# Performance work log

Hardware: AMD Instinct MI355X
Metric: run time of the kernel (lower is better)

The kernel has to match this reference:

```python
import jax, jax.numpy as jnp
import numpy as np

T, B, V, NG, H, MLP = 1024, 128, 128, 10, 1024, 128
F = V + NG  # feature_size = alphabet one-hot + genre one-hot


def setup_inputs() -> dict:
    key = jax.random.key(0)
    ks = jax.random.split(key, 14)
    s = 0.02
    inp = {
        "x": jax.random.normal(ks[0], (T, B, F), dtype=jnp.float32),
        # LSTMCell 1: input F -> hidden H (PyTorch layout: W_ih [4H, F], W_hh [4H, H])
        "W_ih1": jax.random.normal(ks[1], (4 * H, F), dtype=jnp.float32) * s,
        "b_ih1": jax.random.normal(ks[2], (4 * H,), dtype=jnp.float32) * s,
        "W_hh1": jax.random.normal(ks[3], (4 * H, H), dtype=jnp.float32) * s,
        "b_hh1": jax.random.normal(ks[4], (4 * H,), dtype=jnp.float32) * s,
        # LSTMCell 2: H -> H
        "W_ih2": jax.random.normal(ks[5], (4 * H, H), dtype=jnp.float32) * s,
        "b_ih2": jax.random.normal(ks[6], (4 * H,), dtype=jnp.float32) * s,
        "W_hh2": jax.random.normal(ks[7], (4 * H, H), dtype=jnp.float32) * s,
        "b_hh2": jax.random.normal(ks[8], (4 * H,), dtype=jnp.float32) * s,
        # MLP head: Linear(H,128) -> SELU -> Linear(128, V). Dropout(0.2) is identity in eval.
        "W1": jax.random.normal(ks[9], (MLP, H), dtype=jnp.float32) * s,
        "b1": jax.random.normal(ks[10], (MLP,), dtype=jnp.float32) * s,
        "W2": jax.random.normal(ks[11], (V, MLP), dtype=jnp.float32) * s,
        "b2": jax.random.normal(ks[12], (V,), dtype=jnp.float32) * s,
        "predict": 0,
    }
    return inp


def _lstm_cell(xt, h, c, W_ih, b_ih, W_hh, b_hh):
    # PyTorch LSTMCell gate order: input, forget, cell(g), output
    gates = xt @ W_ih.T + b_ih + h @ W_hh.T + b_hh  # [B, 4H]
    i, f, g, o = jnp.split(gates, 4, axis=-1)
    i, f, o = jax.nn.sigmoid(i), jax.nn.sigmoid(f), jax.nn.sigmoid(o)
    g = jnp.tanh(g)
    c_new = f * c + i * g
    h_new = o * jnp.tanh(c_new)
    return h_new, c_new


def reference(x, W_ih1, b_ih1, W_hh1, b_hh1, W_ih2, b_ih2, W_hh2, b_hh2,
              W1, b1, W2, b2, predict):
    n = x.shape[1]
    h0 = jnp.zeros((n, H), dtype=jnp.float32)
    init = (h0, h0, h0, h0)  # h_t, c_t, h2_t, c2_t

    def step(carry, xt):
        h, c, h2, c2 = carry
        h, c = _lstm_cell(xt, h, c, W_ih1, b_ih1, W_hh1, b_hh1)
        h2, c2 = _lstm_cell(h, h2, c2, W_ih2, b_ih2, W_hh2, b_hh2)
        out = jax.nn.selu(h2 @ W1.T + b1) @ W2.T + b2  # [B, V]
        return (h, c, h2, c2), out

    _, outputs = jax.lax.scan(step, init, x)  # [T, B, V]
    return outputs
```

## Files before the change

### kernel.cpp

```cpp
#include <hip/hip_runtime.h>
#include <cstdint>
#include <cstddef>

#define TT   1024
#define BB   128
#define FEAT 138
#define FPAD 160
#define HH   1024
#define VV   128
#define MM   128
#define K1   1184
#define K1P  1280
#define K2   2048
#define HCH  1024
#define H1N  131072
#define MIDN 16384
#define PKM1 1032
#define PKM2 136
#define OFF_RED 0
#define OFF_WM  32768
#define OFF_H   65792
#define OFF_M   67840
#define LDSZ    68864

typedef __bf16 bf16x8 __attribute__((ext_vector_type(8)));
typedef float  f32x4  __attribute__((ext_vector_type(4)));
typedef unsigned short u16;

__device__ __forceinline__ u16 f2bf(float f) {
  uint32_t u = __float_as_uint(f);
  u += 0x7fffu + ((u >> 16) & 1u);
  return (u16)(u >> 16);
}
__device__ __forceinline__ float sigm(float x) { return 1.0f / (1.0f + __expf(-x)); }
__device__ __forceinline__ float tanh_(float x) {
  float e = __expf(-2.0f * fabsf(x));
  float t = (1.0f - e) / (1.0f + e);
  return x < 0.0f ? -t : t;
}

__device__ __forceinline__ bf16x8 ldcc8(const u16* p) {
  union { unsigned long long q[2]; bf16x8 v; } u;
  const unsigned long long* p64 = (const unsigned long long*)p;
  u.q[0] = __hip_atomic_load(p64,     __ATOMIC_RELAXED, __HIP_MEMORY_SCOPE_AGENT);
  u.q[1] = __hip_atomic_load(p64 + 1, __ATOMIC_RELAXED, __HIP_MEMORY_SCOPE_AGENT);
  return u.v;
}
__device__ __forceinline__ void stcc16(u16* p, uint4 v) {
  unsigned long long* p64 = (unsigned long long*)p;
  unsigned long long lo = ((unsigned long long)v.y << 32) | v.x;
  unsigned long long hi = ((unsigned long long)v.w << 32) | v.z;
  __hip_atomic_store(p64,     lo, __ATOMIC_RELAXED, __HIP_MEMORY_SCOPE_AGENT);
  __hip_atomic_store(p64 + 1, hi, __ATOMIC_RELAXED, __HIP_MEMORY_SCOPE_AGENT);
}

__global__ void conv_w1i(const float* __restrict__ Wih, const float* __restrict__ Whh,
                         const float* __restrict__ bi, const float* __restrict__ bh,
                         u16* __restrict__ dst, float* __restrict__ bsum) {
  int rp = blockIdx.x;
  int hc = rp >> 2, g = rp & 3;
  int sr = g * HH + hc;
  if (threadIdx.x == 0) bsum[rp] = bi[sr] + bh[sr];
  for (int k = threadIdx.x; k < K1P; k += 256) {
    float v = 0.0f;
    if (k < FPAD)    v = (k < FEAT) ? Wih[(size_t)sr * FEAT + k] : 0.0f;
    else if (k < K1) v = Whh[(size_t)sr * HH + (k - FPAD)];
    dst[(size_t)rp * K1P + k] = f2bf(v);
  }
}
__global__ void conv_w2i(const float* __restrict__ Wih, const float* __restrict__ Whh,
                         const float* __restrict__ bi, const float* __restrict__ bh,
                         u16* __restrict__ dst, float* __restrict__ bsum) {
  int rp = blockIdx.x;
  int hc = rp >> 2, g = rp & 3;
  int sr = g * HH + hc;
  if (threadIdx.x == 0) bsum[rp] = bi[sr] + bh[sr];
  for (int k = threadIdx.x; k < K2; k += 256) {
    float v = (k < HH) ? Wih[(size_t)sr * HH + k] : Whh[(size_t)sr * HH + (k - HH)];
    dst[(size_t)rp * K2 + k] = f2bf(v);
  }
}
__global__ void conv_mlpw(const float* __restrict__ W1, const float* __restrict__ W2,
                          u16* __restrict__ A, u16* __restrict__ Bm) {
  int i = blockIdx.x * 256 + threadIdx.x;
  if (i < MM * HH) A[i] = f2bf(W1[i]);
  else {
    int j = i - MM * HH;
    if (j < VV * MM) Bm[j] = f2bf(W2[j]);
  }
}
__global__ void conv_x(const float* __restrict__ x, u16* __restrict__ Xb) {
  int blk = blockIdx.x;
  int t = blk / 20, c = blk % 20;
  int b = threadIdx.x;
  if (b >= BB) return;
  const float* src = x + ((size_t)t * BB + b) * FEAT;
  u16 v[8];
#pragma unroll
  for (int e = 0; e < 8; ++e) {
    int col = c * 8 + e;
    v[e] = (col < FEAT) ? f2bf(src[col]) : (u16)0;
  }
  *(uint4*)(Xb + (((size_t)t * 20 + c) * BB + b) * 8) = *(uint4*)v;
}
__global__ void zero_ws(uint4* __restrict__ p, int n16) {
  int i = blockIdx.x * 256 + threadIdx.x;
  if (i < n16) p[i] = uint4{0, 0, 0, 0};
}


__device__ __forceinline__ void mac_step(const bf16x8& a0, const bf16x8& a1,
                                         const u16* __restrict__ bptr,
                                         f32x4 (&acc)[2][4]) {
  bf16x8 Bf[4];
#pragma unroll
  for (int n = 0; n < 4; ++n) Bf[n] = *(const bf16x8*)(bptr + n * 128);
#pragma unroll
  for (int n = 0; n < 4; ++n) {
    acc[0][n] = __builtin_amdgcn_mfma_f32_16x16x32_bf16(a0, Bf[n], acc[0][n], 0, 0, 0);
    acc[1][n] = __builtin_amdgcn_mfma_f32_16x16x32_bf16(a1, Bf[n], acc[1][n], 0, 0, 0);
  }
}

__device__ __forceinline__ void ld_tile_cc(const u16* bptr, bf16x8 (&B)[4]) {
#pragma unroll
  for (int n = 0; n < 4; ++n) B[n] = ldcc8(bptr + n * 128);
}
__device__ __forceinline__ void mfma_tile(const bf16x8& a0, const bf16x8& a1,
                                          const bf16x8 (&B)[4], f32x4 (&acc)[2][4]) {
#pragma unroll
  for (int n = 0; n < 4; ++n) {
    acc[0][n] = __builtin_amdgcn_mfma_f32_16x16x32_bf16(a0, B[n], acc[0][n], 0, 0, 0);
    acc[1][n] = __builtin_amdgcn_mfma_f32_16x16x32_bf16(a1, B[n], acc[1][n], 0, 0, 0);
  }
}
template<int NT, int OFS, int NA>
__device__ __forceinline__ void mac_ring_cc(const bf16x8 (&A0)[NA], const bf16x8 (&A1)[NA],
                                            const u16* __restrict__ bp,
                                            f32x4 (&acc)[2][4]) {
  constexpr int D = NT < 4 ? NT : 4;
  bf16x8 Bq[D][4];
#pragma unroll
  for (int s = 0; s < D; ++s) ld_tile_cc(bp + (size_t)s * 4096, Bq[s]);
#pragma unroll
  for (int s = 0; s < NT; ++s) {
    mfma_tile(A0[OFS + s], A1[OFS + s], Bq[s % D], acc);
    if (s + D < NT) ld_tile_cc(bp + (size_t)(s + D) * 4096, Bq[s % D]);
  }
}

__device__ __forceinline__ void red_write(float* __restrict__ rg,
                                          const f32x4 (&acc)[2][4], int lane) {
#pragma unroll
  for (int mt = 0; mt < 2; ++mt)
#pragma unroll
    for (int n = 0; n < 4; ++n)
      *(f32x4*)(rg + (mt * 4 + n) * 256 + lane * 4) = acc[mt][n];
}
__device__ __forceinline__ void red_add(const float* __restrict__ rg,
                                        f32x4 (&acc)[2][4], int lane) {
#pragma unroll
  for (int mt = 0; mt < 2; ++mt)
#pragma unroll
    for (int n = 0; n < 4; ++n)
      acc[mt][n] += *(const f32x4*)(rg + (mt * 4 + n) * 256 + lane * 4);
}

__device__ __forceinline__ void lstm_tail(f32x4 (&acc)[2][4], const f32x4& bsv0,
                                          const f32x4& bsv1, float (&cst)[2][4],
                                          char* smem, int bh, int lane, int q, int l16,
                                          u16* __restrict__ houtChunk) {
  u16* st = (u16*)(smem + OFF_H) + bh * 512;
#pragma unroll
  for (int mt = 0; mt < 2; ++mt) {
    const f32x4 bsv = mt ? bsv1 : bsv0;
#pragma unroll
    for (int n = 0; n < 4; ++n) {
      float iv = sigm(acc[mt][n][0] + bsv[0]);
      float fv = sigm(acc[mt][n][1] + bsv[1]);
      float gv = tanh_(acc[mt][n][2] + bsv[2]);
      float ov = sigm(acc[mt][n][3] + bsv[3]);
      float c = fv * cst[mt][n] + iv * gv;
      cst[mt][n] = c;
      st[(n * 16 + l16) * 8 + mt * 4 + q] = f2bf(ov * tanh_(c));
    }
  }
  uint4 hv4 = *(uint4*)((u16*)(smem + OFF_H) + bh * 512 + lane * 8);
  stcc16(houtChunk + ((size_t)bh * 64 + lane) * 8, hv4);
}

__device__ __forceinline__ void gbar(unsigned* __restrict__ bar, unsigned g) {
  asm volatile("s_waitcnt vmcnt(0)" ::: "memory");
  __syncthreads();
  if (threadIdx.x == 0) {
    unsigned v = __hip_atomic_fetch_add(&bar[(blockIdx.x & 7) * 16], 1u,
                                        __ATOMIC_RELAXED, __HIP_MEMORY_SCOPE_AGENT);
    if (v == 32u * g - 1u) {
      unsigned w = __hip_atomic_fetch_add(&bar[128], 1u,
                                          __ATOMIC_RELAXED, __HIP_MEMORY_SCOPE_AGENT);
      if (w == 8u * g - 1u)
        __hip_atomic_store(&bar[144], g, __ATOMIC_RELAXED, __HIP_MEMORY_SCOPE_AGENT);
    }
    while (__hip_atomic_load(&bar[144], __ATOMIC_RELAXED,
                             __HIP_MEMORY_SCOPE_AGENT) < g)
      __builtin_amdgcn_s_sleep(8);
  }
  __syncthreads();
}

__global__ __launch_bounds__(512, 2) void fused_lstm(
    const u16* __restrict__ W1i, const u16* __restrict__ W2i,
    const u16* __restrict__ W1m, const u16* __restrict__ W2m,
    const u16* __restrict__ Xb, u16* __restrict__ h1b, u16* __restrict__ h2b,
    u16* __restrict__ midb,
    const float* __restrict__ bs1, const float* __restrict__ bs2,
    const float* __restrict__ bm1, const float* __restrict__ bm2,
    float* __restrict__ out, unsigned* __restrict__ bar)
{
  extern __shared__ char smem[];
  const int tid = threadIdx.x, bid = blockIdx.x;
  const int w = tid >> 6, lane = tid & 63, q = lane >> 4, l16 = lane & 15;
  const int kw = w & 3, bh = w >> 2;
  const bool isL1 = bid < 128;
  const int j = isL1 ? bid : bid - 128;
  float* red = (float*)(smem + OFF_RED);
  u16* Wm = (u16*)(smem + OFF_WM);

  float cst[2][4] = {{0, 0, 0, 0}, {0, 0, 0, 0}};
  f32x4 bsv0 = {0, 0, 0, 0}, bsv1 = {0, 0, 0, 0};
  if (kw == 0) {
    const float* bs = isL1 ? bs1 : bs2;
    bsv0 = *(const f32x4*)(bs + (j * 8 + q) * 4);
    bsv1 = *(const f32x4*)(bs + (j * 8 + 4 + q) * 4);
  }

  if (isL1) {
    bf16x8 A1[2][10];
#pragma unroll
    for (int mt = 0; mt < 2; ++mt)
#pragma unroll
      for (int s = 0; s < 10; ++s)
        A1[mt][s] = *(const bf16x8*)(W1i + (size_t)(j * 32 + mt * 16 + l16) * K1P +
                                     (size_t)(kw * 10 + s) * 32 + q * 8);
    if (j < 64) {
      int m0 = (j & 7) * 16;
      for (int i = tid; i < 16 * 128; i += 512) {
        int r = i >> 7, c8 = i & 127;
        *(uint4*)(Wm + r * PKM1 + c8 * 8) =
            *(const uint4*)(W1m + ((size_t)(m0 + r)) * HH + c8 * 8);
      }
    } else {
      int v0 = ((j - 64) & 7) * 16;
      for (int i = tid; i < 16 * 16; i += 512) {
        int r = i >> 4, c8 = i & 15;
        *(uint4*)(Wm + r * PKM2 + c8 * 8) =
            *(const uint4*)(W2m + ((size_t)(v0 + r)) * MM + c8 * 8);
      }
    }
    f32x4 bmv = {0, 0, 0, 0};
    if (w == 3) {
      if (j < 64) bmv = *(const f32x4*)(bm1 + (j & 7) * 16 + q * 4);
      else        bmv = *(const f32x4*)(bm2 + ((j - 64) & 7) * 16 + q * 4);
    }
    __syncthreads();

    for (int p = 0; p < TT + 3; ++p) {
      const bool act = p < TT;
      if (act) {
        const u16* h1p = h1b + (size_t)((p - 1) & 1) * H1N;
        f32x4 acc[2][4];
#pragma unroll
        for (int mt = 0; mt < 2; ++mt)
#pragma unroll
          for (int n = 0; n < 4; ++n) acc[mt][n] = (f32x4){0, 0, 0, 0};
        if (kw == 0) {
          const u16* bx = Xb + (size_t)p * 20480 +
                          ((size_t)q * 128 + bh * 64 + l16) * 8;
#pragma unroll
          for (int s = 0; s < 5; ++s)
            mac_step(A1[0][s], A1[1][s], bx + (size_t)s * 4096, acc);
          const u16* bp = h1p + ((size_t)q * 128 + bh * 64 + l16) * 8;
          mac_ring_cc<5, 5, 10>(A1[0], A1[1], bp, acc);
        } else {
          const u16* bp = h1p + ((size_t)((kw * 10 - 5) * 4 + q) * 128 +
                                 bh * 64 + l16) * 8;
          mac_ring_cc<10, 0, 10>(A1[0], A1[1], bp, acc);
        }
        if (kw >= 2) red_write(red + (bh * 2 + kw - 2) * 2048, acc, lane);
        __syncthreads();
        if (kw < 2)  red_add(red + (bh * 2 + kw) * 2048, acc, lane);
        if (kw == 1) red_write(red + (bh * 2 + 1) * 2048, acc, lane);
        __syncthreads();
        if (kw == 0) {
          red_add(red + (bh * 2 + 1) * 2048, acc, lane);
          lstm_tail(acc, bsv0, bsv1, cst, smem, bh, lane, q, l16,
                    h1b + (size_t)(p & 1) * H1N + (size_t)j * HCH);
        }
      }
      if (w == 3) {
        if (j < 64) {
          if (p >= 2 && p <= TT + 1) {
            int jm = j & 7, jb = j >> 3;
            const u16* bsrc = h2b + (size_t)(p & 1) * H1N + q * HCH +
                              (jb * 16 + l16) * 8;
            const u16* am = Wm + l16 * PKM1 + q * 8;
            f32x4 acc = {0, 0, 0, 0};
            bf16x8 Bq[8];
#pragma unroll
            for (int s = 0; s < 8; ++s) Bq[s] = ldcc8(bsrc + (size_t)s * 4096);
#pragma unroll
            for (int s = 0; s < 32; ++s) {
              bf16x8 af = *(const bf16x8*)(am + s * 32);
              acc = __builtin_amdgcn_mfma_f32_16x16x32_bf16(af, Bq[s % 8], acc, 0, 0, 0);
              if (s + 8 < 32) Bq[s % 8] = ldcc8(bsrc + (size_t)(s + 8) * 4096);
            }
            const float SC = 1.0507009873554804934193349852946f;
            const float AL = 1.6732632423543772848170429916717f;
            u16* st16 = (u16*)(smem + OFF_M);
#pragma unroll
            for (int r = 0; r < 4; ++r) {
              float v = acc[r] + bmv[r];
              v = v > 0.0f ? SC * v : SC * AL * (__expf(v) - 1.0f);
              st16[l16 * 16 + q * 4 + r] = f2bf(v);
            }
            if (lane < 16) {
              uint4 v0 = *(uint4*)(st16 + lane * 16);
              uint4 v1 = *(uint4*)(st16 + lane * 16 + 8);
              u16* mc = midb + (size_t)(p & 1) * MIDN;
              stcc16(mc + (size_t)(2 * jm) * HCH + (jb * 16 + lane) * 8, v0);
              stcc16(mc + (size_t)(2 * jm + 1) * HCH + (jb * 16 + lane) * 8, v1);
            }
          }
        } else if (p >= 3) {
          int jj = j - 64, jv = jj & 7, jb = jj >> 3;
          const u16* bsrc = midb + (size_t)((p - 3) & 1) * MIDN + q * HCH +
                            (jb * 16 + l16) * 8;
          const u16* am = Wm + l16 * PKM2 + q * 8;
          f32x4 acc = {0, 0, 0, 0};
          bf16x8 Bq[4];
#pragma unroll
          for (int s = 0; s < 4; ++s) Bq[s] = ldcc8(bsrc + (size_t)s * 4096);
#pragma unroll
          for (int s = 0; s < 4; ++s) {
            bf16x8 af = *(const bf16x8*)(am + s * 32);
            acc = __builtin_amdgcn_mfma_f32_16x16x32_bf16(af, Bq[s], acc, 0, 0, 0);
          }
          float* stf = (float*)(smem + OFF_M);
#pragma unroll
          for (int r = 0; r < 4; ++r) stf[l16 * 16 + q * 4 + r] = acc[r] + bmv[r];
          if (lane < 16) {
            float* orow = out + ((size_t)(p - 3) * BB + jb * 16 + lane) * VV + jv * 16;
            uint4* s4 = (uint4*)(stf + lane * 16);
            *(uint4*)(orow + 0)  = s4[0];
            *(uint4*)(orow + 4)  = s4[1];
            *(uint4*)(orow + 8)  = s4[2];
            *(uint4*)(orow + 12) = s4[3];
          }
        }
      }
      gbar(bar, (unsigned)p + 1u);
    }
  } else {
    bf16x8 A2[2][16];
#pragma unroll
    for (int mt = 0; mt < 2; ++mt)
#pragma unroll
      for (int s = 0; s < 16; ++s)
        A2[mt][s] = *(const bf16x8*)(W2i + (size_t)(j * 32 + mt * 16 + l16) * K2 +
                                     (size_t)(kw * 16 + s) * 32 + q * 8);

    for (int p = 0; p < TT + 3; ++p) {
      const bool act = (p >= 1 && p <= TT);
      if (act) {
        const int t = p - 1;
        const u16* h1c = h1b + (size_t)(t & 1) * H1N;
        const u16* h2p = h2b + (size_t)((t - 1) & 1) * H1N;
        const u16* src = (kw < 2) ? h1c : h2p;
        const u16* bbase = src + ((size_t)((kw & 1) * 64 + q) * 128 +
                                  bh * 64 + l16) * 8;
        f32x4 acc[2][4];
#pragma unroll
        for (int mt = 0; mt < 2; ++mt)
#pragma unroll
          for (int n = 0; n < 4; ++n) acc[mt][n] = (f32x4){0, 0, 0, 0};
        mac_ring_cc<16, 0, 16>(A2[0], A2[1], bbase, acc);

        if (kw >= 2) red_write(red + (bh * 2 + kw - 2) * 2048, acc, lane);
        __syncthreads();
        if (kw < 2)  red_add(red + (bh * 2 + kw) * 2048, acc, lane);
        if (kw == 1) red_write(red + (bh * 2 + 1) * 2048, acc, lane);
        __syncthreads();
        if (kw == 0) {
          red_add(red + (bh * 2 + 1) * 2048, acc, lane);
          lstm_tail(acc, bsv0, bsv1, cst, smem, bh, lane, q, l16,
                    h2b + (size_t)(t & 1) * H1N + (size_t)j * HCH);
        }
      }
      gbar(bar, (unsigned)p + 1u);
    }
  }
}

extern "C" void kernel_launch(void* const* d_in, const int* in_sizes, int n_in,
                              void* d_out, int out_size, void* d_ws, size_t ws_size,
                              hipStream_t stream)
{
  const float* x    = (const float*)d_in[0];
  const float* Wih1 = (const float*)d_in[1];
  const float* bih1 = (const float*)d_in[2];
  const float* Whh1 = (const float*)d_in[3];
  const float* bhh1 = (const float*)d_in[4];
  const float* Wih2 = (const float*)d_in[5];
  const float* bih2 = (const float*)d_in[6];
  const float* Whh2 = (const float*)d_in[7];
  const float* bhh2 = (const float*)d_in[8];
  const float* W1   = (const float*)d_in[9];
  const float* b1   = (const float*)d_in[10];
  const float* W2   = (const float*)d_in[11];
  const float* b2   = (const float*)d_in[12];
  float* out = (float*)d_out;
  (void)in_sizes; (void)n_in; (void)out_size;

  char* ws = (char*)d_ws;
  size_t off = 0;
  auto alloc = [&](size_t n) { char* p = ws + off; off += (n + 255) & ~(size_t)255; return p; };
  u16* W1i   = (u16*)alloc((size_t)4096 * K1P * 2);
  u16* W2i   = (u16*)alloc((size_t)4096 * K2 * 2);
  u16* W1m   = (u16*)alloc((size_t)MM * HH * 2);
  u16* W2m   = (u16*)alloc((size_t)VV * MM * 2);
  u16* Xb    = (u16*)alloc((size_t)TT * 20 * BB * 8 * 2);
  float* bs1 = (float*)alloc(4096 * 4);
  float* bs2 = (float*)alloc(4096 * 4);
  u16* h1b   = (u16*)alloc(2 * (size_t)H1N * 2 + 32768);
  u16* h2b   = (u16*)alloc(2 * (size_t)H1N * 2);
  u16* midb  = (u16*)alloc(2 * (size_t)MIDN * 2);
  unsigned* bar = (unsigned*)alloc(4096);
  if (ws_size < off) return;

  conv_w1i<<<4096, 256, 0, stream>>>(Wih1, Whh1, bih1, bhh1, W1i, bs1);
  conv_w2i<<<4096, 256, 0, stream>>>(Wih2, Whh2, bih2, bhh2, W2i, bs2);
  conv_mlpw<<<576, 256, 0, stream>>>(W1, W2, W1m, W2m);
  conv_x<<<TT * 20, 128, 0, stream>>>(x, Xb);
  {
    int n16 = (int)((2 * (size_t)H1N * 2 + 32768 + 2 * (size_t)H1N * 2 +
                     2 * (size_t)MIDN * 2 + 4096) / 16);
    zero_ws<<<(n16 + 255) / 256, 256, 0, stream>>>((uint4*)h1b, n16);
  }

  (void)hipFuncSetAttribute((const void*)fused_lstm,
                            hipFuncAttributeMaxDynamicSharedMemorySize, LDSZ);
  void* args[] = { (void*)&W1i, (void*)&W2i, (void*)&W1m, (void*)&W2m,
                   (void*)&Xb, (void*)&h1b, (void*)&h2b, (void*)&midb,
                   (void*)&bs1, (void*)&bs2, (void*)&b1, (void*)&b2,
                   (void*)&out, (void*)&bar };
  hipError_t err = hipLaunchCooperativeKernel((const void*)fused_lstm,
                                              dim3(256), dim3(512), args, LDSZ, stream);
  if (err != hipSuccess) {
    fused_lstm<<<dim3(256), dim3(512), LDSZ, stream>>>(W1i, W2i, W1m, W2m, Xb,
                                                       h1b, h2b, midb, bs1, bs2,
                                                       b1, b2, out, bar);
  }
}
```

Before: 16.16 ms.

## Replace grid barrier with per-block flag wait over deep ring buffers

Adds a MODE 4 path that replaces the two-level atomic grid barrier with per-block completion flags. Every block polls all 256 flags before each phase, and an acquire fence is issued only once every 128 phases, staggered per block. Hidden-state and MLP intermediate buffers become 256-deep rings with padded strides. Reads that used to be coherent atomic loads become plain vector loads, relying on fresh ring slots so stale cache lines are not hit. The cost is much more workspace, and correctness now depends on the ring depth and the sparse fences. Layer-1 blocks with kw==3 also skip padded K tiles, and the barrier sleep is shortened.

```diff
diff --git a/kernel.cpp b/kernel.cpp
--- a/kernel.cpp
+++ b/kernel.cpp
@@ -15,6 +15,9 @@
 #define HCH  1024
 #define H1N  131072
 #define MIDN 16384
+#define H1S  135168
+#define MIDS 20480
+#define RING 256
 #define PKM1 1032
 #define PKM2 136
 #define OFF_RED 0
@@ -39,13 +42,6 @@
   return x < 0.0f ? -t : t;
 }
 
-__device__ __forceinline__ bf16x8 ldcc8(const u16* p) {
-  union { unsigned long long q[2]; bf16x8 v; } u;
-  const unsigned long long* p64 = (const unsigned long long*)p;
-  u.q[0] = __hip_atomic_load(p64,     __ATOMIC_RELAXED, __HIP_MEMORY_SCOPE_AGENT);
-  u.q[1] = __hip_atomic_load(p64 + 1, __ATOMIC_RELAXED, __HIP_MEMORY_SCOPE_AGENT);
-  return u.v;
-}
 __device__ __forceinline__ void stcc16(u16* p, uint4 v) {
   unsigned long long* p64 = (unsigned long long*)p;
   unsigned long long lo = ((unsigned long long)v.y << 32) | v.x;
@@ -109,23 +105,6 @@
 }
 
 
-__device__ __forceinline__ void mac_step(const bf16x8& a0, const bf16x8& a1,
-                                         const u16* __restrict__ bptr,
-                                         f32x4 (&acc)[2][4]) {
-  bf16x8 Bf[4];
-#pragma unroll
-  for (int n = 0; n < 4; ++n) Bf[n] = *(const bf16x8*)(bptr + n * 128);
-#pragma unroll
-  for (int n = 0; n < 4; ++n) {
-    acc[0][n] = __builtin_amdgcn_mfma_f32_16x16x32_bf16(a0, Bf[n], acc[0][n], 0, 0, 0);
-    acc[1][n] = __builtin_amdgcn_mfma_f32_16x16x32_bf16(a1, Bf[n], acc[1][n], 0, 0, 0);
-  }
-}
-
-__device__ __forceinline__ void ld_tile_cc(const u16* bptr, bf16x8 (&B)[4]) {
-#pragma unroll
-  for (int n = 0; n < 4; ++n) B[n] = ldcc8(bptr + n * 128);
-}
 __device__ __forceinline__ void mfma_tile(const bf16x8& a0, const bf16x8& a1,
                                           const bf16x8 (&B)[4], f32x4 (&acc)[2][4]) {
 #pragma unroll
@@ -134,18 +113,22 @@
     acc[1][n] = __builtin_amdgcn_mfma_f32_16x16x32_bf16(a1, B[n], acc[1][n], 0, 0, 0);
   }
 }
+__device__ __forceinline__ void ld_tile(const u16* __restrict__ p, bf16x8 (&B)[4]) {
+#pragma unroll
+  for (int n = 0; n < 4; ++n) B[n] = *(const bf16x8*)(p + n * 128);
+}
 template<int NT, int OFS, int NA>
-__device__ __forceinline__ void mac_ring_cc(const bf16x8 (&A0)[NA], const bf16x8 (&A1)[NA],
-                                            const u16* __restrict__ bp,
-                                            f32x4 (&acc)[2][4]) {
+__device__ __forceinline__ void mac_ring(const bf16x8 (&A0)[NA], const bf16x8 (&A1)[NA],
+                                         const u16* __restrict__ bp,
+                                         f32x4 (&acc)[2][4]) {
   constexpr int D = NT < 4 ? NT : 4;
   bf16x8 Bq[D][4];
 #pragma unroll
-  for (int s = 0; s < D; ++s) ld_tile_cc(bp + (size_t)s * 4096, Bq[s]);
+  for (int s = 0; s < D; ++s) ld_tile(bp + (size_t)s * 4096, Bq[s]);
 #pragma unroll
   for (int s = 0; s < NT; ++s) {
     mfma_tile(A0[OFS + s], A1[OFS + s], Bq[s % D], acc);
-    if (s + D < NT) ld_tile_cc(bp + (size_t)(s + D) * 4096, Bq[s % D]);
+    if (s + D < NT) ld_tile(bp + (size_t)(s + D) * 4096, Bq[s % D]);
   }
 }
 
@@ -187,6 +170,30 @@
   }
   uint4 hv4 = *(uint4*)((u16*)(smem + OFF_H) + bh * 512 + lane * 8);
   stcc16(houtChunk + ((size_t)bh * 64 + lane) * 8, hv4);
+}
+
+template<int MODE>
+__device__ __forceinline__ void wait_phase(const int* __restrict__ F, int p, int lane,
+                                           bool dofence) {
+  if (threadIdx.x < 64) {
+    if (dofence)
+      __builtin_amdgcn_fence(__ATOMIC_ACQUIRE, "agent");
+    for (;;) {
+      int a = __hip_atomic_load(F + lane,       __ATOMIC_RELAXED, __HIP_MEMORY_SCOPE_AGENT);
+      int b = __hip_atomic_load(F + 64 + lane,  __ATOMIC_RELAXED, __HIP_MEMORY_SCOPE_AGENT);
+      int c = __hip_atomic_load(F + 128 + lane, __ATOMIC_RELAXED, __HIP_MEMORY_SCOPE_AGENT);
+      int d = __hip_atomic_load(F + 192 + lane, __ATOMIC_RELAXED, __HIP_MEMORY_SCOPE_AGENT);
+      if (__all(a >= p && b >= p && c >= p && d >= p)) break;
+      __builtin_amdgcn_s_sleep(1);
+    }
+  }
+  __syncthreads();
+}
+__device__ __forceinline__ void done_phase(int* __restrict__ slot, int p) {
+  asm volatile("s_waitcnt vmcnt(0)" ::: "memory");
+  __syncthreads();
+  if (threadIdx.x == 0)
+    __hip_atomic_store(slot, p + 1, __ATOMIC_RELAXED, __HIP_MEMORY_SCOPE_AGENT);
 }
 
 __device__ __forceinline__ void gbar(unsigned* __restrict__ bar, unsigned g) {
@@ -201,14 +208,16 @@
       if (w == 8u * g - 1u)
         __hip_atomic_store(&bar[144], g, __ATOMIC_RELAXED, __HIP_MEMORY_SCOPE_AGENT);
     }
+    __builtin_amdgcn_fence(__ATOMIC_ACQUIRE, "agent");
     while (__hip_atomic_load(&bar[144], __ATOMIC_RELAXED,
                              __HIP_MEMORY_SCOPE_AGENT) < g)
-      __builtin_amdgcn_s_sleep(8);
+      __builtin_amdgcn_s_sleep(1);
   }
   __syncthreads();
 }
 
-__global__ __launch_bounds__(512, 2) void fused_lstm(
+template<int MODE>
+__global__ __launch_bounds__(512) void fused_lstm(
     const u16* __restrict__ W1i, const u16* __restrict__ W2i,
     const u16* __restrict__ W1m, const u16* __restrict__ W2m,
     const u16* __restrict__ Xb, u16* __restrict__ h1b, u16* __restrict__ h2b,
@@ -225,6 +234,12 @@
   const int j = isL1 ? bid : bid - 128;
   float* red = (float*)(smem + OFF_RED);
   u16* Wm = (u16*)(smem + OFF_WM);
+  int* flags = (int*)bar;
+  constexpr int    HRM = (MODE == 4) ? (RING - 1) : 1;
+  constexpr size_t HST = (MODE == 4) ? H1S : H1N;
+  constexpr int    MRM = (MODE == 4) ? (RING - 1) : 1;
+  constexpr size_t MST = (MODE == 4) ? MIDS : MIDN;
+  const unsigned boff = (unsigned)(bid * 37u) & 127u;
 
   float cst[2][4] = {{0, 0, 0, 0}, {0, 0, 0, 0}};
   f32x4 bsv0 = {0, 0, 0, 0}, bsv1 = {0, 0, 0, 0};
@@ -242,6 +257,7 @@
       for (int s = 0; s < 10; ++s)
         A1[mt][s] = *(const bf16x8*)(W1i + (size_t)(j * 32 + mt * 16 + l16) * K1P +
                                      (size_t)(kw * 10 + s) * 32 + q * 8);
+    f32x4 bmv = {0, 0, 0, 0};
     if (j < 64) {
       int m0 = (j & 7) * 16;
       for (int i = tid; i < 16 * 128; i += 512) {
@@ -257,7 +273,6 @@
             *(const uint4*)(W2m + ((size_t)(v0 + r)) * MM + c8 * 8);
       }
     }
-    f32x4 bmv = {0, 0, 0, 0};
     if (w == 3) {
       if (j < 64) bmv = *(const f32x4*)(bm1 + (j & 7) * 16 + q * 4);
       else        bmv = *(const f32x4*)(bm2 + ((j - 64) & 7) * 16 + q * 4);
@@ -265,9 +280,11 @@
     __syncthreads();
 
     for (int p = 0; p < TT + 3; ++p) {
+      if constexpr (MODE == 4)
+        wait_phase<MODE>(flags, p, lane, (((unsigned)p + boff) & 127u) == 0u);
       const bool act = p < TT;
       if (act) {
-        const u16* h1p = h1b + (size_t)((p - 1) & 1) * H1N;
+        const u16* h1p = h1b + (size_t)((p - 1) & HRM) * HST;
         f32x4 acc[2][4];
 #pragma unroll
         for (int mt = 0; mt < 2; ++mt)
@@ -276,15 +293,14 @@
         if (kw == 0) {
           const u16* bx = Xb + (size_t)p * 20480 +
                           ((size_t)q * 128 + bh * 64 + l16) * 8;
-#pragma unroll
-          for (int s = 0; s < 5; ++s)
-            mac_step(A1[0][s], A1[1][s], bx + (size_t)s * 4096, acc);
+          mac_ring<5, 0, 10>(A1[0], A1[1], bx, acc);
           const u16* bp = h1p + ((size_t)q * 128 + bh * 64 + l16) * 8;
-          mac_ring_cc<5, 5, 10>(A1[0], A1[1], bp, acc);
+          mac_ring<5, 5, 10>(A1[0], A1[1], bp, acc);
         } else {
           const u16* bp = h1p + ((size_t)((kw * 10 - 5) * 4 + q) * 128 +
                                  bh * 64 + l16) * 8;
-          mac_ring_cc<10, 0, 10>(A1[0], A1[1], bp, acc);
+          if (kw == 3) mac_ring<7, 0, 10>(A1[0], A1[1], bp, acc);
+          else         mac_ring<10, 0, 10>(A1[0], A1[1], bp, acc);
         }
         if (kw >= 2) red_write(red + (bh * 2 + kw - 2) * 2048, acc, lane);
         __syncthreads();
@@ -294,25 +310,25 @@
         if (kw == 0) {
           red_add(red + (bh * 2 + 1) * 2048, acc, lane);
           lstm_tail(acc, bsv0, bsv1, cst, smem, bh, lane, q, l16,
-                    h1b + (size_t)(p & 1) * H1N + (size_t)j * HCH);
+                    h1b + (size_t)(p & HRM) * HST + (size_t)j * HCH);
         }
       }
       if (w == 3) {
         if (j < 64) {
           if (p >= 2 && p <= TT + 1) {
             int jm = j & 7, jb = j >> 3;
-            const u16* bsrc = h2b + (size_t)(p & 1) * H1N + q * HCH +
+            const u16* bsrc = h2b + (size_t)((p - 2) & HRM) * HST + q * HCH +
                               (jb * 16 + l16) * 8;
             const u16* am = Wm + l16 * PKM1 + q * 8;
             f32x4 acc = {0, 0, 0, 0};
             bf16x8 Bq[8];
 #pragma unroll
-            for (int s = 0; s < 8; ++s) Bq[s] = ldcc8(bsrc + (size_t)s * 4096);
+            for (int s = 0; s < 8; ++s) Bq[s] = *(const bf16x8*)(bsrc + (size_t)s * 4096);
 #pragma unroll
             for (int s = 0; s < 32; ++s) {
               bf16x8 af = *(const bf16x8*)(am + s * 32);
               acc = __builtin_amdgcn_mfma_f32_16x16x32_bf16(af, Bq[s % 8], acc, 0, 0, 0);
-              if (s + 8 < 32) Bq[s % 8] = ldcc8(bsrc + (size_t)(s + 8) * 4096);
+              if (s + 8 < 32) Bq[s % 8] = *(const bf16x8*)(bsrc + (size_t)(s + 8) * 4096);
             }
             const float SC = 1.0507009873554804934193349852946f;
             const float AL = 1.6732632423543772848170429916717f;
@@ -326,24 +342,22 @@
             if (lane < 16) {
               uint4 v0 = *(uint4*)(st16 + lane * 16);
               uint4 v1 = *(uint4*)(st16 + lane * 16 + 8);
-              u16* mc = midb + (size_t)(p & 1) * MIDN;
+              u16* mc = midb + (size_t)((p - 2) & MRM) * MST;
               stcc16(mc + (size_t)(2 * jm) * HCH + (jb * 16 + lane) * 8, v0);
               stcc16(mc + (size_t)(2 * jm + 1) * HCH + (jb * 16 + lane) * 8, v1);
             }
           }
         } else if (p >= 3) {
           int jj = j - 64, jv = jj & 7, jb = jj >> 3;
-          const u16* bsrc = midb + (size_t)((p - 3) & 1) * MIDN + q * HCH +
+          const u16* bsrc = midb + (size_t)((p - 3) & MRM) * MST + q * HCH +
                             (jb * 16 + l16) * 8;
           const u16* am = Wm + l16 * PKM2 + q * 8;
           f32x4 acc = {0, 0, 0, 0};
-          bf16x8 Bq[4];
-#pragma unroll
-          for (int s = 0; s < 4; ++s) Bq[s] = ldcc8(bsrc + (size_t)s * 4096);
 #pragma unroll
           for (int s = 0; s < 4; ++s) {
+            bf16x8 bf = *(const bf16x8*)(bsrc + (size_t)s * 4096);
             bf16x8 af = *(const bf16x8*)(am + s * 32);
-            acc = __builtin_amdgcn_mfma_f32_16x16x32_bf16(af, Bq[s], acc, 0, 0, 0);
+            acc = __builtin_amdgcn_mfma_f32_16x16x32_bf16(af, bf, acc, 0, 0, 0);
           }
           float* stf = (float*)(smem + OFF_M);
 #pragma unroll
@@ -358,7 +372,8 @@
           }
         }
       }
-      gbar(bar, (unsigned)p + 1u);
+      if constexpr (MODE == 0) gbar(bar, (unsigned)p + 1u);
+      else                     done_phase(flags + bid, p);
     }
   } else {
     bf16x8 A2[2][16];
@@ -370,11 +385,13 @@
                                      (size_t)(kw * 16 + s) * 32 + q * 8);
 
     for (int p = 0; p < TT + 3; ++p) {
+      if constexpr (MODE == 4)
+        wait_phase<MODE>(flags, p, lane, (((unsigned)p + boff) & 127u) == 0u);
       const bool act = (p >= 1 && p <= TT);
       if (act) {
         const int t = p - 1;
-        const u16* h1c = h1b + (size_t)(t & 1) * H1N;
-        const u16* h2p = h2b + (size_t)((t - 1) & 1) * H1N;
+        const u16* h1c = h1b + (size_t)(t & HRM) * HST;
+        const u16* h2p = h2b + (size_t)((t - 1) & HRM) * HST;
         const u16* src = (kw < 2) ? h1c : h2p;
         const u16* bbase = src + ((size_t)((kw & 1) * 64 + q) * 128 +
                                   bh * 64 + l16) * 8;
@@ -383,7 +400,7 @@
         for (int mt = 0; mt < 2; ++mt)
 #pragma unroll
           for (int n = 0; n < 4; ++n) acc[mt][n] = (f32x4){0, 0, 0, 0};
-        mac_ring_cc<16, 0, 16>(A2[0], A2[1], bbase, acc);
+        mac_ring<16, 0, 16>(A2[0], A2[1], bbase, acc);
 
         if (kw >= 2) red_write(red + (bh * 2 + kw - 2) * 2048, acc, lane);
         __syncthreads();
@@ -393,10 +410,11 @@
         if (kw == 0) {
           red_add(red + (bh * 2 + 1) * 2048, acc, lane);
           lstm_tail(acc, bsv0, bsv1, cst, smem, bh, lane, q, l16,
-                    h2b + (size_t)(t & 1) * H1N + (size_t)j * HCH);
+                    h2b + (size_t)(t & HRM) * HST + (size_t)j * HCH);
         }
       }
-      gbar(bar, (unsigned)p + 1u);
+      if constexpr (MODE == 0) gbar(bar, (unsigned)p + 1u);
+      else                     done_phase(flags + bid, p);
     }
   }
 }
@@ -431,11 +449,17 @@
   u16* Xb    = (u16*)alloc((size_t)TT * 20 * BB * 8 * 2);
   float* bs1 = (float*)alloc(4096 * 4);
   float* bs2 = (float*)alloc(4096 * 4);
-  u16* h1b   = (u16*)alloc(2 * (size_t)H1N * 2 + 32768);
-  u16* h2b   = (u16*)alloc(2 * (size_t)H1N * 2);
-  u16* midb  = (u16*)alloc(2 * (size_t)MIDN * 2);
+  u16* h1bF  = (u16*)alloc(2 * (size_t)H1N * 2 + 32768);
+  u16* h2bF  = (u16*)alloc(2 * (size_t)H1N * 2);
+  u16* midbF = (u16*)alloc(2 * (size_t)MIDN * 2);
   unsigned* bar = (unsigned*)alloc(4096);
-  if (ws_size < off) return;
+  size_t off_base = off;
+  u16* h1r   = (u16*)alloc((size_t)RING * H1S * 2);
+  u16* h2r   = (u16*)alloc((size_t)RING * H1S * 2);
+  u16* midr  = (u16*)alloc((size_t)RING * MIDS * 2);
+  size_t off_m4 = off;
+  int mode = (ws_size >= off_m4) ? 4 : 0;
+  if (ws_size < off_base) return;
 
   conv_w1i<<<4096, 256, 0, stream>>>(Wih1, Whh1, bih1, bhh1, W1i, bs1);
   conv_w2i<<<4096, 256, 0, stream>>>(Wih2, Whh2, bih2, bhh2, W2i, bs2);
@@ -444,20 +468,37 @@
   {
     int n16 = (int)((2 * (size_t)H1N * 2 + 32768 + 2 * (size_t)H1N * 2 +
                      2 * (size_t)MIDN * 2 + 4096) / 16);
-    zero_ws<<<(n16 + 255) / 256, 256, 0, stream>>>((uint4*)h1b, n16);
-  }
-
-  (void)hipFuncSetAttribute((const void*)fused_lstm,
+    zero_ws<<<(n16 + 255) / 256, 256, 0, stream>>>((uint4*)h1bF, n16);
+  }
+  if (mode == 4) {
+    zero_ws<<<(H1N * 2 / 16 + 255) / 256, 256, 0, stream>>>(
+        (uint4*)(h1r + (size_t)(RING - 1) * H1S), H1N * 2 / 16);
+    zero_ws<<<(H1N * 2 / 16 + 255) / 256, 256, 0, stream>>>(
+        (uint4*)(h2r + (size_t)(RING - 1) * H1S), H1N * 2 / 16);
+  }
+
+  u16* h1p = (mode == 4) ? h1r : h1bF;
+  u16* h2p = (mode == 4) ? h2r : h2bF;
+  u16* mdp = (mode == 4) ? midr : midbF;
+
+  using KFn = void (*)(const u16*, const u16*, const u16*, const u16*, const u16*,
+                       u16*, u16*, u16*, const float*, const float*,
+                       const float*, const float*, float*, unsigned*);
+  KFn fp = (mode == 4) ? (KFn)fused_lstm<4> : (KFn)fused_lstm<0>;
+  (void)hipFuncSetAttribute((const void*)fp,
                             hipFuncAttributeMaxDynamicSharedMemorySize, LDSZ);
   void* args[] = { (void*)&W1i, (void*)&W2i, (void*)&W1m, (void*)&W2m,
-                   (void*)&Xb, (void*)&h1b, (void*)&h2b, (void*)&midb,
+                   (void*)&Xb, (void*)&h1p, (void*)&h2p, (void*)&mdp,
                    (void*)&bs1, (void*)&bs2, (void*)&b1, (void*)&b2,
                    (void*)&out, (void*)&bar };
-  hipError_t err = hipLaunchCooperativeKernel((const void*)fused_lstm,
+  hipError_t err = hipLaunchCooperativeKernel((const void*)fp,
                                               dim3(256), dim3(512), args, LDSZ, stream);
   if (err != hipSuccess) {
-    fused_lstm<<<dim3(256), dim3(512), LDSZ, stream>>>(W1i, W2i, W1m, W2m, Xb,
-                                                       h1b, h2b, midb, bs1, bs2,
-                                                       b1, b2, out, bar);
-  }
-}
+    if (mode == 4)
+      fused_lstm<4><<<dim3(256), dim3(512), LDSZ, stream>>>(
+          W1i, W2i, W1m, W2m, Xb, h1p, h2p, mdp, bs1, bs2, b1, b2, out, bar);
+    else
+      fused_lstm<0><<<dim3(256), dim3(512), LDSZ, stream>>>(
+          W1i, W2i, W1m, W2m, Xb, h1p, h2p, mdp, bs1, bs2, b1, b2, out, bar);
+  }
+}
```

Result: faster. 15.73 ms (-2.7%).
